# Optimization experiments

Hardware: AMD Instinct MI355X
Metric: run time of the kernel (lower is better)

The kernel has to match this reference:

```python
import jax, jax.numpy as jnp
import numpy as np

IMAGE_SIZE = 224
PATCH_SIZE = 16
HALF_PATCH = PATCH_SIZE // 2
GRID = IMAGE_SIZE // PATCH_SIZE  # 14
NUM_PATCHES = GRID * GRID        # 196
C_IN = 3
C_CAT = 5 * C_IN                 # 15
PATCH_DIM = PATCH_SIZE * PATCH_SIZE * C_CAT  # 3840
PROJ_DIM = 768
EPS = 1e-6


def setup_inputs() -> dict:
    key = jax.random.key(0)
    k1, k2 = jax.random.split(key)
    images = jax.random.normal(k1, (64, IMAGE_SIZE, IMAGE_SIZE, C_IN), dtype=jnp.float32)
    W = jax.random.normal(k2, (PATCH_DIM, PROJ_DIM), dtype=jnp.float32) * 0.02
    b = jnp.zeros((PROJ_DIM,), dtype=jnp.float32)
    gamma = jnp.ones((PATCH_DIM,), dtype=jnp.float32)
    beta = jnp.zeros((PATCH_DIM,), dtype=jnp.float32)
    return {"images": images, "gamma": gamma, "beta": beta, "W": W, "b": b}


def _shift(images, crop_h, crop_w, shift_h, shift_w):
    S, hp = IMAGE_SIZE, HALF_PATCH
    # crop to (S-hp, S-hp) at (crop_h, crop_w), then pad back to (S, S) at (shift_h, shift_w)
    crop = images[:, crop_h:crop_h + S - hp, crop_w:crop_w + S - hp, :]
    return jnp.pad(crop, ((0, 0), (shift_h, hp - shift_h), (shift_w, hp - shift_w), (0, 0)))


def _forward(images, gamma, beta, W, b):
    hp = HALF_PATCH
    x = jnp.concatenate([
        images,
        _shift(images, hp, hp, 0, 0),   # left-up
        _shift(images, 0, hp, hp, 0),   # left-down
        _shift(images, hp, 0, 0, hp),   # right-up
        _shift(images, 0, 0, hp, hp),   # right-down
    ], axis=-1)  # [B, S, S, 15]
    B = x.shape[0]
    # non-overlapping patch extraction (tf.image.extract_patches, VALID, stride=patch)
    patches = (x.reshape(B, GRID, PATCH_SIZE, GRID, PATCH_SIZE, C_CAT)
                 .transpose(0, 1, 3, 2, 4, 5)
                 .reshape(B, GRID, GRID, PATCH_DIM))  # [B, 14, 14, 3840]
    flat = patches.reshape(B, NUM_PATCHES, PATCH_DIM)
    mean = jnp.mean(flat, axis=-1, keepdims=True)
    var = jnp.mean(jnp.square(flat - mean), axis=-1, keepdims=True)
    normed = (flat - mean) * jax.lax.rsqrt(var + EPS) * gamma + beta
    tokens = jnp.einsum('bnd,de->bne', normed, W) + b  # [B, 196, 768]
    return tokens, patches


def reference(images, gamma, beta, W, b):
    return _forward(images, gamma, beta, W, b)
```

## Files before the change

kernel.cpp:

```cpp
#include <hip/hip_runtime.h>
#include <hip/hip_bf16.h>

typedef unsigned short u16;
typedef unsigned int   u32;
typedef __attribute__((ext_vector_type(8))) short short8;
typedef __attribute__((ext_vector_type(4))) float floatx4;

#define IMG      224
#define GRIDD    14
#define NPATCH   12544
#define KDIM     3840
#define PROJ     768
#define MW_BLOCKS 2880
#define BK       64
#define NKT      (KDIM / BK)
#define TILE_B   (128 * BK * 2)


__device__ __forceinline__ float b2f(u16 u) {
  union { u32 i; float f; } x; x.i = ((u32)u) << 16; return x.f;
}
__device__ __forceinline__ u16 f2b(float f) {
  union { u32 i; float f; } x; x.f = f;
  u32 r = x.i + 0x7fffu + ((x.i >> 16) & 1u);
  return (u16)(r >> 16);
}

__device__ __forceinline__ bool probe_bf16(const void* gamma) {
  return *(const u32*)gamma == 0x3F803F80u;
}
__device__ __forceinline__ float ldin(const void* p, size_t i, bool bf) {
  return bf ? b2f(((const u16*)p)[i]) : ((const float*)p)[i];
}

__device__ __forceinline__ void async_copy16(void* lds_uniform_base, const void* g) {
  __builtin_amdgcn_global_load_lds((const __attribute__((address_space(1))) u32*)g,
                                   (__attribute__((address_space(3))) u32*)lds_uniform_base,
                                   16, 0, 0);
}

struct alignas(8) us4 { u16 x, y, z, w; };

__device__ __forceinline__ int tile_swz_byte(int r, int bc) {
  return r * 128 + (((bc & ~15) ^ ((r & 7) << 4)) + (bc & 15));
}

__global__ __launch_bounds__(256) void prep(const void* __restrict__ W,
                                            const void* __restrict__ gamma,
                                            const void* __restrict__ beta,
                                            u16* __restrict__ Wgt,
                                            float* __restrict__ u_arr,
                                            float* __restrict__ v_arr,
                                            const void* __restrict__ images,
                                            void* __restrict__ d_out,
                                            float2* __restrict__ meaninv,
                                            u16* __restrict__ Abf) {
  const bool bf = probe_bf16(gamma);
  const int tid = threadIdx.x;

  if (blockIdx.x < MW_BLOCKS) {
    __shared__ u16 tile[32][33];
    __shared__ float gs[32], bs[32];
    __shared__ float pu[8][33], pv[8][33];
    const int blk = blockIdx.x;
    const int bx = blk % 24;
    const int by = blk / 24;
    const int tx = tid & 31;
    const int ty = tid >> 5;
    if (ty == 0) {
      gs[tx] = ldin(gamma, by * 32 + tx, bf);
      bs[tx] = ldin(beta,  by * 32 + tx, bf);
    }
    __syncthreads();
    float ut = 0.f, vt = 0.f;
#pragma unroll
    for (int j = 0; j < 4; ++j) {
      const int a = ty + j * 8;
      const float wf = ldin(W, (size_t)(by * 32 + a) * PROJ + bx * 32 + tx, bf);
      ut += gs[a] * wf;
      vt += bs[a] * wf;
      tile[a][tx] = f2b(gs[a] * wf);
    }
    pu[ty][tx] = ut; pv[ty][tx] = vt;
    __syncthreads();
    if (ty == 0) {
      float su = 0.f, sv = 0.f;
#pragma unroll
      for (int t = 0; t < 8; ++t) { su += pu[t][tx]; sv += pv[t][tx]; }
      atomicAdd(&u_arr[bx * 32 + tx], su);
      atomicAdd(&v_arr[bx * 32 + tx], sv);
    }
#pragma unroll
    for (int j = 0; j < 4; ++j) {
      const int n  = bx * 32 + ty + j * 8;
      const int k  = by * 32 + tx;
      const int cb = n >> 7, nr = n & 127;
      const int kt = k >> 6, bc = (k & 63) * 2;
      const size_t off = (size_t)(cb * NKT + kt) * 8192 + (tile_swz_byte(nr, bc) >> 1);
      Wgt[off] = tile[tx][ty + j * 8];
    }
    return;
  }

  const int p   = blockIdx.x - MW_BLOCKS;
  const int b   = p / 196;
  const int rem = p - b * 196;
  const int gy  = rem / GRIDD;
  const int gx  = rem - gy * GRIDD;

  __shared__ alignas(16) float buf[KDIM];
  __shared__ float red_s[4], red_q[4];

  {
    const int h0  = gy * 16 - 8;
    const int wc0 = gx * 48 - 24;
#pragma unroll
    for (int k = 0; k < 12; ++k) {
      const int f    = tid + k * 256;
      const int t1   = f >> 5;
      const int rrow = (t1 * 43691) >> 17;
      const int colf = f - rrow * 96;
      const int h    = h0 + rrow;
      const int wc   = wc0 + colf;
      const bool ok  = (h >= 0) && (h < IMG) && (wc >= 0) && (wc < IMG * 3);
      buf[f] = ok ? ldin(images, (size_t)(b * IMG + h) * (IMG * 3) + wc, bf) : 0.f;
    }
  }
  __syncthreads();

  const int py = tid >> 4, px = tid & 15;
  const int rbase = (py + 8) * 96 + (px + 8) * 3;
  const int goff[5] = {0, 792, -744, 744, -792};
  float r[15];
  float s = 0.f, q = 0.f;
#pragma unroll
  for (int g = 0; g < 5; ++g)
#pragma unroll
    for (int c = 0; c < 3; ++c) {
      const float f = buf[rbase + goff[g] + c];
      r[g * 3 + c] = f;
      s += f; q += f * f;
    }
  __syncthreads();

#pragma unroll
  for (int j = 0; j < 15; ++j) buf[tid * 15 + j] = r[j];

#pragma unroll
  for (int off = 32; off > 0; off >>= 1) {
    s += __shfl_down(s, off);
    q += __shfl_down(q, off);
  }
  const int wave = tid >> 6, lane = tid & 63;
  if (lane == 0) { red_s[wave] = s; red_q[wave] = q; }
  __syncthreads();

  const float S = red_s[0] + red_s[1] + red_s[2] + red_s[3];
  const float Q = red_q[0] + red_q[1] + red_q[2] + red_q[3];
  const float mean = S * (1.f / (float)KDIM);
  const float var  = Q * (1.f / (float)KDIM) - mean * mean;
  const float inv  = rsqrtf(var + 1e-6f);
  if (tid == 0) meaninv[p] = make_float2(mean, inv);

  const size_t pb = (size_t)p * KDIM;
  const int    mr = p & 127;
  const size_t tb = (size_t)(p >> 7) * NKT * 8192;
  if (bf) {
    u16* po = (u16*)d_out + (size_t)NPATCH * PROJ;
    for (int i = tid; i < KDIM / 4; i += 256) {
      const int d = i * 4;
      us4 o;
      o.x = f2b(buf[d + 0]); o.y = f2b(buf[d + 1]);
      o.z = f2b(buf[d + 2]); o.w = f2b(buf[d + 3]);
      *(us4*)&po[pb + d] = o;
      if (Abf) {
        const int kt = d >> 6, bc = (d & 63) * 2;
        *(us4*)&Abf[tb + (size_t)kt * 8192 + (tile_swz_byte(mr, bc) >> 1)] = o;
      }
    }
  } else {
    float* po = (float*)d_out + (size_t)NPATCH * PROJ;
    for (int i = tid; i < KDIM / 4; i += 256) {
      const int d = i * 4;
      const float4 v = *(const float4*)&buf[d];
      *(float4*)&po[pb + d] = v;
      if (Abf) {
        us4 o;
        o.x = f2b(v.x); o.y = f2b(v.y); o.z = f2b(v.z); o.w = f2b(v.w);
        const int kt = d >> 6, bc = (d & 63) * 2;
        *(us4*)&Abf[tb + (size_t)kt * 8192 + (tile_swz_byte(mr, bc) >> 1)] = o;
      }
    }
  }
}

__global__ __launch_bounds__(256) void gemm_ln_bf(const u16* __restrict__ Abf,
                                                  const u16* __restrict__ Wgt,
                                                  const float2* __restrict__ meaninv,
                                                  const float* __restrict__ u_arr,
                                                  const float* __restrict__ v_arr,
                                                  const void* __restrict__ bias,
                                                  const void* __restrict__ gamma,
                                                  void* __restrict__ d_out) {
  const bool bf = probe_bf16(gamma);
  __shared__ alignas(16) u16 As[128 * BK];
  __shared__ alignas(16) u16 Bs[128 * BK];
  __shared__ float2 mi[128];

  const int tid  = threadIdx.x;
  const int wave = tid >> 6, lane = tid & 63;
  const int cb = blockIdx.x;
  const int rb = blockIdx.y;

  const int m0 = (wave >> 1) * 64;
  const int n0 = (wave & 1) * 64;
  const int lr = lane & 15, quad = lane >> 4;

  if (tid < 128) mi[tid] = meaninv[rb * 128 + tid];

  floatx4 acc[4][4];
#pragma unroll
  for (int i = 0; i < 4; ++i)
#pragma unroll
    for (int j = 0; j < 4; ++j)
      acc[i][j] = (floatx4)0.f;

  const char* Ab = (const char*)Abf + (size_t)rb * NKT * TILE_B;
  const char* Bb = (const char*)Wgt + (size_t)cb * NKT * TILE_B;
  const int lane16 = lane * 16;

  for (int kt = 0; kt < NKT; ++kt) {
    __syncthreads();
    const size_t tb = (size_t)kt * TILE_B;
#pragma unroll
    for (int pass = 0; pass < 4; ++pass) {
      const int s_ = pass * 4 + wave;
      async_copy16((char*)As + s_ * 1024, Ab + tb + s_ * 1024 + lane16);
      async_copy16((char*)Bs + s_ * 1024, Bb + tb + s_ * 1024 + lane16);
    }
    __syncthreads();

#pragma unroll
    for (int s = 0; s < 2; ++s) {
      short8 af[4], bfr[4];
      const int u = (s * 4 + quad) ^ (lr & 7);
#pragma unroll
      for (int i = 0; i < 4; ++i)
        af[i] = *(const short8*)&As[(m0 + i * 16 + lr) * BK + u * 8];
#pragma unroll
      for (int j = 0; j < 4; ++j)
        bfr[j] = *(const short8*)&Bs[(n0 + j * 16 + lr) * BK + u * 8];
#pragma unroll
      for (int i = 0; i < 4; ++i)
#pragma unroll
        for (int j = 0; j < 4; ++j)
          acc[i][j] = __builtin_amdgcn_mfma_f32_16x16x32_bf16(af[i], bfr[j], acc[i][j], 0, 0, 0);
    }
  }

#pragma unroll
  for (int j = 0; j < 4; ++j) {
    const int col = cb * 128 + n0 + j * 16 + lr;
    const float uc = u_arr[col];
    const float vc = v_arr[col] + ldin(bias, col, bf);
#pragma unroll
    for (int i = 0; i < 4; ++i) {
      const int rl0 = m0 + i * 16 + quad * 4;
#pragma unroll
      for (int t = 0; t < 4; ++t) {
        const float2 m = mi[rl0 + t];
        const float val = m.y * (acc[i][j][t] - m.x * uc) + vc;
        const size_t idx = (size_t)(rb * 128 + rl0 + t) * PROJ + col;
        if (bf) ((u16*)d_out)[idx] = f2b(val);
        else    ((float*)d_out)[idx] = val;
      }
    }
  }
}

__global__ __launch_bounds__(256) void gemm_ln_fp(const void* __restrict__ gamma,
                                                  const u16* __restrict__ Wgt,
                                                  const float2* __restrict__ meaninv,
                                                  const float* __restrict__ u_arr,
                                                  const float* __restrict__ v_arr,
                                                  const void* __restrict__ bias,
                                                  void* __restrict__ d_out) {
  const bool bf = probe_bf16(gamma);
  __shared__ alignas(16) u16 As[128 * BK];
  __shared__ alignas(16) u16 Bs[128 * BK];
  __shared__ float2 mi[128];

  const int tid  = threadIdx.x;
  const int wave = tid >> 6, lane = tid & 63;
  const int cb = blockIdx.x;
  const int rb = blockIdx.y;
  const int m0 = (wave >> 1) * 64;
  const int n0 = (wave & 1) * 64;
  const int lr = lane & 15, quad = lane >> 4;

  if (tid < 128) mi[tid] = meaninv[rb * 128 + tid];

  floatx4 acc[4][4];
#pragma unroll
  for (int i = 0; i < 4; ++i)
#pragma unroll
    for (int j = 0; j < 4; ++j)
      acc[i][j] = (floatx4)0.f;

  const char* patches2 = (const char*)d_out + (size_t)NPATCH * PROJ * 2;
  const char* patches4 = (const char*)d_out + (size_t)NPATCH * PROJ * 4;
  const char* Bb  = (const char*)Wgt + (size_t)cb * NKT * TILE_B;

  for (int kt = 0; kt < NKT; ++kt) {
    __syncthreads();
#pragma unroll
    for (int c = 0; c < 4; ++c) {
      const int o = c * 4096 + tid * 16;
      *(uint4*)((char*)Bs + o) = *(const uint4*)(Bb + (size_t)kt * TILE_B + o);
    }
#pragma unroll
    for (int c = 0; c < 4; ++c) {
      const int t  = c * 256 + tid;
      const int r  = t >> 3;
      const int u  = (t & 7) ^ (r & 7);
      const int d0 = kt * BK + u * 8;
      union { uint4 qv; u16 hv[8]; } pk;
      if (bf) {
        pk.qv = *(const uint4*)(patches2 + (size_t)(rb * 128 + r) * (KDIM * 2) + d0 * 2);
      } else {
        const char* ga = patches4 + (size_t)(rb * 128 + r) * (KDIM * 4) + d0 * 4;
        const float4 f0 = *(const float4*)ga;
        const float4 f1 = *(const float4*)(ga + 16);
        pk.hv[0] = f2b(f0.x); pk.hv[1] = f2b(f0.y); pk.hv[2] = f2b(f0.z); pk.hv[3] = f2b(f0.w);
        pk.hv[4] = f2b(f1.x); pk.hv[5] = f2b(f1.y); pk.hv[6] = f2b(f1.z); pk.hv[7] = f2b(f1.w);
      }
      *(uint4*)((char*)As + t * 16) = pk.qv;
    }
    __syncthreads();

#pragma unroll
    for (int s = 0; s < 2; ++s) {
      short8 af[4], bfr[4];
      const int u = (s * 4 + quad) ^ (lr & 7);
#pragma unroll
      for (int i = 0; i < 4; ++i)
        af[i] = *(const short8*)&As[(m0 + i * 16 + lr) * BK + u * 8];
#pragma unroll
      for (int j = 0; j < 4; ++j)
        bfr[j] = *(const short8*)&Bs[(n0 + j * 16 + lr) * BK + u * 8];
#pragma unroll
      for (int i = 0; i < 4; ++i)
#pragma unroll
        for (int j = 0; j < 4; ++j)
          acc[i][j] = __builtin_amdgcn_mfma_f32_16x16x32_bf16(af[i], bfr[j], acc[i][j], 0, 0, 0);
    }
  }

#pragma unroll
  for (int j = 0; j < 4; ++j) {
    const int col = cb * 128 + n0 + j * 16 + lr;
    const float uc = u_arr[col];
    const float vc = v_arr[col] + ldin(bias, col, bf);
#pragma unroll
    for (int i = 0; i < 4; ++i) {
      const int rl0 = m0 + i * 16 + quad * 4;
#pragma unroll
      for (int t = 0; t < 4; ++t) {
        const float2 m = mi[rl0 + t];
        const float val = m.y * (acc[i][j][t] - m.x * uc) + vc;
        const size_t idx = (size_t)(rb * 128 + rl0 + t) * PROJ + col;
        if (bf) ((u16*)d_out)[idx] = f2b(val);
        else    ((float*)d_out)[idx] = val;
      }
    }
  }
}

extern "C" void kernel_launch(void* const* d_in, const int* in_sizes, int n_in,
                              void* d_out, int out_size, void* d_ws, size_t ws_size,
                              hipStream_t stream) {
  (void)in_sizes; (void)n_in; (void)out_size;
  const void* images = d_in[0];
  const void* gamma  = d_in[1];
  const void* beta   = d_in[2];
  const void* W      = d_in[3];
  const void* bias   = d_in[4];

  u16*    Wgt     = (u16*)d_ws;
  size_t  off     = (size_t)PROJ * KDIM * 2;
  float2* meaninv = (float2*)((char*)d_ws + off);
  off            += (size_t)NPATCH * 8;
  float*  u_arr   = (float*)((char*)d_ws + off);
  off            += PROJ * 4;
  float*  v_arr   = (float*)((char*)d_ws + off);
  off            += PROJ * 4;
  u16*    Abf     = (u16*)((char*)d_ws + off);
  const size_t need = off + (size_t)NPATCH * KDIM * 2;
  const bool useA = ws_size >= need;

  hipMemsetAsync(u_arr, 0, 2 * PROJ * sizeof(float), stream);
  hipLaunchKernelGGL(prep, dim3(MW_BLOCKS + NPATCH), dim3(256), 0, stream,
                     W, gamma, beta, Wgt, u_arr, v_arr,
                     images, d_out, meaninv, useA ? Abf : (u16*)nullptr);
  if (useA)
    hipLaunchKernelGGL(gemm_ln_bf, dim3(6, 98), dim3(256), 0, stream,
                       Abf, Wgt, meaninv, u_arr, v_arr, bias, gamma, d_out);
  else
    hipLaunchKernelGGL(gemm_ln_fp, dim3(6, 98), dim3(256), 0, stream,
                       gamma, Wgt, meaninv, u_arr, v_arr, bias, d_out);
}
```

Before: 485.4 us.

## Double-buffer GEMM LDS tiles with async prefetch and remap blocks across XCDs

```diff
diff --git a/kernel.cpp b/kernel.cpp
--- a/kernel.cpp
+++ b/kernel.cpp
@@ -203,20 +203,28 @@
                                                   const void* __restrict__ gamma,
                                                   void* __restrict__ d_out) {
   const bool bf = probe_bf16(gamma);
-  __shared__ alignas(16) u16 As[128 * BK];
-  __shared__ alignas(16) u16 Bs[128 * BK];
+  __shared__ alignas(16) u16 As0[128 * BK];
+  __shared__ alignas(16) u16 Bs0[128 * BK];
+  __shared__ alignas(16) u16 As1[128 * BK];
+  __shared__ alignas(16) u16 Bs1[128 * BK];
   __shared__ float2 mi[128];
 
   const int tid  = threadIdx.x;
   const int wave = tid >> 6, lane = tid & 63;
-  const int cb = blockIdx.x;
-  const int rb = blockIdx.y;
+
+  const int lin  = blockIdx.y * 6 + blockIdx.x;
+  const int xcd  = lin & 7;
+  const int slot = lin >> 3;
+  const int v    = (xcd < 4 ? xcd * 74 : 296 + (xcd - 4) * 73) + slot;
+  const int rb   = v / 6;
+  const int cb   = v - rb * 6;
 
   const int m0 = (wave >> 1) * 64;
   const int n0 = (wave & 1) * 64;
   const int lr = lane & 15, quad = lane >> 4;
 
   if (tid < 128) mi[tid] = meaninv[rb * 128 + tid];
+  __syncthreads();
 
   floatx4 acc[4][4];
 #pragma unroll
@@ -229,34 +237,67 @@
   const char* Bb = (const char*)Wgt + (size_t)cb * NKT * TILE_B;
   const int lane16 = lane * 16;
 
-  for (int kt = 0; kt < NKT; ++kt) {
-    __syncthreads();
-    const size_t tb = (size_t)kt * TILE_B;
-#pragma unroll
-    for (int pass = 0; pass < 4; ++pass) {
-      const int s_ = pass * 4 + wave;
-      async_copy16((char*)As + s_ * 1024, Ab + tb + s_ * 1024 + lane16);
-      async_copy16((char*)Bs + s_ * 1024, Bb + tb + s_ * 1024 + lane16);
-    }
-    __syncthreads();
-
-#pragma unroll
-    for (int s = 0; s < 2; ++s) {
-      short8 af[4], bfr[4];
-      const int u = (s * 4 + quad) ^ (lr & 7);
-#pragma unroll
-      for (int i = 0; i < 4; ++i)
-        af[i] = *(const short8*)&As[(m0 + i * 16 + lr) * BK + u * 8];
-#pragma unroll
-      for (int j = 0; j < 4; ++j)
-        bfr[j] = *(const short8*)&Bs[(n0 + j * 16 + lr) * BK + u * 8];
-#pragma unroll
-      for (int i = 0; i < 4; ++i)
-#pragma unroll
-        for (int j = 0; j < 4; ++j)
-          acc[i][j] = __builtin_amdgcn_mfma_f32_16x16x32_bf16(af[i], bfr[j], acc[i][j], 0, 0, 0);
-    }
-  }
+#define STAGE(Ad, Bd, kt)                                                       \
+  {                                                                             \
+    const size_t tb_ = (size_t)(kt) * TILE_B;                                   \
+    _Pragma("unroll")                                                           \
+    for (int pass = 0; pass < 4; ++pass) {                                      \
+      const int s_ = pass * 4 + wave;             \
+      async_copy16((char*)(Ad) + s_ * 1024, Ab + tb_ + s_ * 1024 + lane16);     \
+      async_copy16((char*)(Bd) + s_ * 1024, Bb + tb_ + s_ * 1024 + lane16);     \
+    }                                                                           \
+  }
+
+#define COMPUTE(Asrc, Bsrc)                                                     \
+  {                                                                             \
+    _Pragma("unroll")                                                           \
+    for (int s = 0; s < 2; ++s) {              \
+      short8 af[4], bfr[4];                                                     \
+      const int u = (s * 4 + quad) ^ (lr & 7);           \
+      _Pragma("unroll")                                                         \
+      for (int i = 0; i < 4; ++i)                                               \
+        af[i] = *(const short8*)&(Asrc)[(m0 + i * 16 + lr) * BK + u * 8];       \
+      _Pragma("unroll")                                                         \
+      for (int j = 0; j < 4; ++j)                                               \
+        bfr[j] = *(const short8*)&(Bsrc)[(n0 + j * 16 + lr) * BK + u * 8];      \
+      _Pragma("unroll")                                                         \
+      for (int i = 0; i < 4; ++i)                                               \
+        _Pragma("unroll")                                                       \
+        for (int j = 0; j < 4; ++j)                                             \
+          acc[i][j] = __builtin_amdgcn_mfma_f32_16x16x32_bf16(af[i], bfr[j],    \
+                                                             acc[i][j], 0,0,0);\
+    }                                                                           \
+  }
+
+#define VMW8()  asm volatile("s_waitcnt vmcnt(8)" ::: "memory")
+#define VMW0()  asm volatile("s_waitcnt vmcnt(0)" ::: "memory")
+#define LGKM0() asm volatile("s_waitcnt lgkmcnt(0)" ::: "memory")
+#define BARR()  asm volatile("s_barrier" ::: "memory")
+
+  STAGE(As0, Bs0, 0);
+  STAGE(As1, Bs1, 1);
+
+  for (int kt = 0; kt < NKT - 2; kt += 2) {
+    VMW8(); BARR();
+    COMPUTE(As0, Bs0);
+    LGKM0(); BARR();
+    STAGE(As0, Bs0, kt + 2);
+    VMW8(); BARR();
+    COMPUTE(As1, Bs1);
+    LGKM0(); BARR();
+    STAGE(As1, Bs1, kt + 3);
+  }
+  VMW8(); BARR();
+  COMPUTE(As0, Bs0);
+  VMW0(); BARR();
+  COMPUTE(As1, Bs1);
+
+#undef STAGE
+#undef COMPUTE
+#undef VMW8
+#undef VMW0
+#undef LGKM0
+#undef BARR
 
 #pragma unroll
   for (int j = 0; j < 4; ++j) {
```

Result: faster. 455.3 us (-6.2%).
